# Optimization experiments

Hardware: AMD Instinct MI355X
Metric: run time of the kernel (lower is better)

The kernel has to match this reference:

```python
import jax, jax.numpy as jnp
import numpy as np

DIS_Z = 0.5     # depth search half-window (init kwarg dis_z)
NSAMPLE = 64    # max neighbors per query (init kwarg nsample)
B, N, M = 8, 16384, 2048


def setup_inputs() -> dict:
    key = jax.random.key(0)
    k1, k2 = jax.random.split(key)
    xyz1 = jax.random.normal(k1, (B, 3, N), dtype=jnp.float32)  # input points
    xyz2 = jax.random.normal(k2, (B, 3, M), dtype=jnp.float32)  # query points
    return {"xyz1": xyz1, "xyz2": xyz2}


def reference(xyz1, xyz2):
    """Depth-constrained radius search (semantics of query_depth_point CUDA kernel).

    For each query point q, scan input points j in order; if |z_j - z_q| < dis_z,
    record j. The first match pre-fills all nsample slots (ball-query convention),
    then subsequent matches overwrite slots 1..nsample-1. Stops after nsample
    matches. Returns idx (B,M,nsample) int64 and pts_cnt (B,M) int32.
    """
    n = xyz1.shape[2]
    z1 = xyz1[:, 2, :]                    # [B, N] input-point depths
    z2 = xyz2[:, 2, :]                    # [B, M] query-point depths
    # [B, M, N] depth-window mask (only the z coordinate is compared)
    mask = jnp.abs(z2[:, :, None] - z1[:, None, :]) < DIS_Z
    # Score earlier indices higher so top_k returns the FIRST nsample matches
    # in scan order; non-matches score 0.
    score = jnp.where(mask, n - jnp.arange(n, dtype=jnp.int32), 0)  # [B, M, N]
    vals, _ = jax.lax.top_k(score, NSAMPLE)   # [B, M, nsample], descending
    valid = vals > 0                          # slot k has a real (k-th) match
    idx_raw = n - vals                        # recover original index where valid
    first = idx_raw[..., 0:1]                 # index of first match (if any)
    cnt_total = jnp.sum(mask, axis=-1)        # [B, M] total matches
    pts_cnt = jnp.minimum(cnt_total, NSAMPLE).astype(jnp.int32)
    # Unfilled slots hold the first match index; if no match at all, stay 0.
    idx = jnp.where(valid, idx_raw,
                    jnp.where(cnt_total[..., None] > 0, first, 0)).astype(jnp.int64)
    return idx, pts_cnt
```

## Files before the change

kernel.cpp:

```cpp
#include <hip/hip_runtime.h>


#define QDP_B 8
#define QDP_N 16384
#define QDP_M 2048
#define QDP_NS 64
#define QDP_DISZ 0.5f

__global__ __launch_bounds__(256) void QueryDepthPoint_kernel(
    const float* __restrict__ xyz1,
    const float* __restrict__ xyz2,
    int* __restrict__ out_idx,
    int* __restrict__ out_cnt)
{
    const int lane = threadIdx.x & 63;
    const int wid  = (blockIdx.x << 2) + (threadIdx.x >> 6);

    const int b = wid >> 11;
    const int q = wid & (QDP_M - 1);

    const float zq = xyz2[b * 3 * QDP_M + 2 * QDP_M + q];
    const float* __restrict__ z1 = xyz1 + b * 3 * QDP_N + 2 * QDP_N;
    int* __restrict__ idx_out = out_idx + (size_t)wid * QDP_NS;

    int cnt    = 0;
    int firstv = 0;
    const unsigned long long below = (1ull << lane) - 1ull;

    const float* lptr = z1 + 8 * lane;
    float4 curA = ((const float4*)lptr)[0];
    float4 curB = ((const float4*)lptr)[1];

    for (int c = 0; c < QDP_N; c += 512) {
        const int pc = (c + 512 < QDP_N) ? (c + 512) : 0;
        const float* nptr = z1 + pc + 8 * lane;
        float4 nxtA = ((const float4*)nptr)[0];
        float4 nxtB = ((const float4*)nptr)[1];

        const bool m0 = fabsf(curA.x - zq) < QDP_DISZ;
        const bool m1 = fabsf(curA.y - zq) < QDP_DISZ;
        const bool m2 = fabsf(curA.z - zq) < QDP_DISZ;
        const bool m3 = fabsf(curA.w - zq) < QDP_DISZ;
        const bool m4 = fabsf(curB.x - zq) < QDP_DISZ;
        const bool m5 = fabsf(curB.y - zq) < QDP_DISZ;
        const bool m6 = fabsf(curB.z - zq) < QDP_DISZ;
        const bool m7 = fabsf(curB.w - zq) < QDP_DISZ;

        const unsigned long long b0 = __ballot(m0);
        const unsigned long long b1 = __ballot(m1);
        const unsigned long long b2 = __ballot(m2);
        const unsigned long long b3 = __ballot(m3);
        const unsigned long long b4 = __ballot(m4);
        const unsigned long long b5 = __ballot(m5);
        const unsigned long long b6 = __ballot(m6);
        const unsigned long long b7 = __ballot(m7);
        const unsigned long long any = b0|b1|b2|b3|b4|b5|b6|b7;

        if (any) {
            const int mbyte = (int)m0 | ((int)m1<<1) | ((int)m2<<2) | ((int)m3<<3)
                            | ((int)m4<<4) | ((int)m5<<5) | ((int)m6<<6) | ((int)m7<<7);
            if (cnt == 0) {
                const int l0  = (int)__builtin_ctzll(any);
                const int mb0 = __shfl(mbyte, l0);
                firstv = c + 8 * l0 + (int)__builtin_ctz((unsigned)mb0);
            }
            int r = cnt + __popcll(b0 & below) + __popcll(b1 & below)
                        + __popcll(b2 & below) + __popcll(b3 & below)
                        + __popcll(b4 & below) + __popcll(b5 & below)
                        + __popcll(b6 & below) + __popcll(b7 & below);
            const int base = c + 8 * lane;
            if (m0) { if (r < QDP_NS) idx_out[r] = base + 0; r++; }
            if (m1) { if (r < QDP_NS) idx_out[r] = base + 1; r++; }
            if (m2) { if (r < QDP_NS) idx_out[r] = base + 2; r++; }
            if (m3) { if (r < QDP_NS) idx_out[r] = base + 3; r++; }
            if (m4) { if (r < QDP_NS) idx_out[r] = base + 4; r++; }
            if (m5) { if (r < QDP_NS) idx_out[r] = base + 5; r++; }
            if (m6) { if (r < QDP_NS) idx_out[r] = base + 6; r++; }
            if (m7) { if (r < QDP_NS) idx_out[r] = base + 7; r++; }
            cnt += __popcll(b0) + __popcll(b1) + __popcll(b2) + __popcll(b3)
                 + __popcll(b4) + __popcll(b5) + __popcll(b6) + __popcll(b7);
            if (cnt >= QDP_NS) { cnt = QDP_NS; break; }
        }
        curA = nxtA; curB = nxtB;
    }

    if (lane >= cnt) idx_out[lane] = firstv;
    if (lane == 0)   out_cnt[wid] = cnt;
}

extern "C" void kernel_launch(void* const* d_in, const int* in_sizes, int n_in,
                              void* d_out, int out_size, void* d_ws, size_t ws_size,
                              hipStream_t stream) {
    const float* xyz1 = (const float*)d_in[0];
    const float* xyz2 = (const float*)d_in[1];
    int* out = (int*)d_out;

    int* out_idx = out;
    int* out_cnt = out + (size_t)QDP_B * QDP_M * QDP_NS;

    const int total_waves = QDP_B * QDP_M;
    const int grid = total_waves / 4;

    QueryDepthPoint_kernel<<<grid, 256, 0, stream>>>(xyz1, xyz2, out_idx, out_cnt);
}
```

Measured before the change: 72.76 us.

## Process sixteen queries per wavefront with a persistent grid and batched loads

Each wavefront now handles 16 consecutive queries in sequence instead of one. The grid shrinks to 256 blocks, and query depths are loaded once per wave and broadcast with shuffles. The scan loads four 512-element chunks per iteration before testing them, replacing the one-ahead prefetch. This cuts launch and wave setup overhead, but serializes queries within a wave and reduces parallelism to 1024 waves. That may leave the GPU underoccupied and expose load latency.

```diff
diff --git a/kernel.cpp b/kernel.cpp
--- a/kernel.cpp
+++ b/kernel.cpp
@@ -6,6 +6,56 @@
 #define QDP_M 2048
 #define QDP_NS 64
 #define QDP_DISZ 0.5f
+#define QDP_QPW 16
+
+__device__ __forceinline__ void qdp_group(
+    int cg, float zq, const float4& A, const float4& B,
+    int lane, unsigned long long below,
+    int& cnt, int& firstv, int* __restrict__ idx_out)
+{
+    const bool m0 = fabsf(A.x - zq) < QDP_DISZ;
+    const bool m1 = fabsf(A.y - zq) < QDP_DISZ;
+    const bool m2 = fabsf(A.z - zq) < QDP_DISZ;
+    const bool m3 = fabsf(A.w - zq) < QDP_DISZ;
+    const bool m4 = fabsf(B.x - zq) < QDP_DISZ;
+    const bool m5 = fabsf(B.y - zq) < QDP_DISZ;
+    const bool m6 = fabsf(B.z - zq) < QDP_DISZ;
+    const bool m7 = fabsf(B.w - zq) < QDP_DISZ;
+
+    const unsigned long long b0 = __ballot(m0);
+    const unsigned long long b1 = __ballot(m1);
+    const unsigned long long b2 = __ballot(m2);
+    const unsigned long long b3 = __ballot(m3);
+    const unsigned long long b4 = __ballot(m4);
+    const unsigned long long b5 = __ballot(m5);
+    const unsigned long long b6 = __ballot(m6);
+    const unsigned long long b7 = __ballot(m7);
+    const unsigned long long any = b0|b1|b2|b3|b4|b5|b6|b7;
+    if (!any) return;
+
+    const int mbyte = (int)m0 | ((int)m1<<1) | ((int)m2<<2) | ((int)m3<<3)
+                    | ((int)m4<<4) | ((int)m5<<5) | ((int)m6<<6) | ((int)m7<<7);
+    if (cnt == 0) {
+        const int l0  = (int)__builtin_ctzll(any);
+        const int mb0 = __shfl(mbyte, l0);
+        firstv = cg + 8 * l0 + (int)__builtin_ctz((unsigned)mb0);
+    }
+    int r = cnt + __popcll(b0 & below) + __popcll(b1 & below)
+                + __popcll(b2 & below) + __popcll(b3 & below)
+                + __popcll(b4 & below) + __popcll(b5 & below)
+                + __popcll(b6 & below) + __popcll(b7 & below);
+    const int base = cg + 8 * lane;
+    if (m0) { if (r < QDP_NS) idx_out[r] = base + 0; r++; }
+    if (m1) { if (r < QDP_NS) idx_out[r] = base + 1; r++; }
+    if (m2) { if (r < QDP_NS) idx_out[r] = base + 2; r++; }
+    if (m3) { if (r < QDP_NS) idx_out[r] = base + 3; r++; }
+    if (m4) { if (r < QDP_NS) idx_out[r] = base + 4; r++; }
+    if (m5) { if (r < QDP_NS) idx_out[r] = base + 5; r++; }
+    if (m6) { if (r < QDP_NS) idx_out[r] = base + 6; r++; }
+    if (m7) { if (r < QDP_NS) idx_out[r] = base + 7; r++; }
+    cnt += __popcll(b0) + __popcll(b1) + __popcll(b2) + __popcll(b3)
+         + __popcll(b4) + __popcll(b5) + __popcll(b6) + __popcll(b7);
+}
 
 __global__ __launch_bounds__(256) void QueryDepthPoint_kernel(
     const float* __restrict__ xyz1,
@@ -14,78 +64,48 @@
     int* __restrict__ out_cnt)
 {
     const int lane = threadIdx.x & 63;
-    const int wid  = (blockIdx.x << 2) + (threadIdx.x >> 6);
-
-    const int b = wid >> 11;
-    const int q = wid & (QDP_M - 1);
-
-    const float zq = xyz2[b * 3 * QDP_M + 2 * QDP_M + q];
-    const float* __restrict__ z1 = xyz1 + b * 3 * QDP_N + 2 * QDP_N;
-    int* __restrict__ idx_out = out_idx + (size_t)wid * QDP_NS;
-
-    int cnt    = 0;
-    int firstv = 0;
+    const int wv   = (blockIdx.x << 2) + (threadIdx.x >> 6);
     const unsigned long long below = (1ull << lane) - 1ull;
 
-    const float* lptr = z1 + 8 * lane;
-    float4 curA = ((const float4*)lptr)[0];
-    float4 curB = ((const float4*)lptr)[1];
+    const int qbase = wv * QDP_QPW;
+    const int b = qbase >> 11;
+    const float* __restrict__ z1 = xyz1 + b * 3 * QDP_N + 2 * QDP_N;
+    const float* __restrict__ z2 = xyz2 + b * 3 * QDP_M + 2 * QDP_M;
 
-    for (int c = 0; c < QDP_N; c += 512) {
-        const int pc = (c + 512 < QDP_N) ? (c + 512) : 0;
-        const float* nptr = z1 + pc + 8 * lane;
-        float4 nxtA = ((const float4*)nptr)[0];
-        float4 nxtB = ((const float4*)nptr)[1];
+    const float zqv = z2[(qbase & (QDP_M - 1)) + (lane & (QDP_QPW - 1))];
 
-        const bool m0 = fabsf(curA.x - zq) < QDP_DISZ;
-        const bool m1 = fabsf(curA.y - zq) < QDP_DISZ;
-        const bool m2 = fabsf(curA.z - zq) < QDP_DISZ;
-        const bool m3 = fabsf(curA.w - zq) < QDP_DISZ;
-        const bool m4 = fabsf(curB.x - zq) < QDP_DISZ;
-        const bool m5 = fabsf(curB.y - zq) < QDP_DISZ;
-        const bool m6 = fabsf(curB.z - zq) < QDP_DISZ;
-        const bool m7 = fabsf(curB.w - zq) < QDP_DISZ;
+    #pragma unroll 1
+    for (int k = 0; k < QDP_QPW; ++k) {
+        const float zq = __shfl(zqv, k);
+        int* __restrict__ idx_out = out_idx + (size_t)(qbase + k) * QDP_NS;
+        int cnt = 0, firstv = 0;
 
-        const unsigned long long b0 = __ballot(m0);
-        const unsigned long long b1 = __ballot(m1);
-        const unsigned long long b2 = __ballot(m2);
-        const unsigned long long b3 = __ballot(m3);
-        const unsigned long long b4 = __ballot(m4);
-        const unsigned long long b5 = __ballot(m5);
-        const unsigned long long b6 = __ballot(m6);
-        const unsigned long long b7 = __ballot(m7);
-        const unsigned long long any = b0|b1|b2|b3|b4|b5|b6|b7;
+        #pragma unroll 1
+        for (int c = 0; c < QDP_N; c += 2048) {
+            const float* p = z1 + c + 8 * lane;
+            const float4 a0 = ((const float4*)p)[0];
+            const float4 b0 = ((const float4*)p)[1];
+            const float4 a1 = ((const float4*)(p + 512))[0];
+            const float4 b1 = ((const float4*)(p + 512))[1];
+            const float4 a2 = ((const float4*)(p + 1024))[0];
+            const float4 b2 = ((const float4*)(p + 1024))[1];
+            const float4 a3 = ((const float4*)(p + 1536))[0];
+            const float4 b3 = ((const float4*)(p + 1536))[1];
 
-        if (any) {
-            const int mbyte = (int)m0 | ((int)m1<<1) | ((int)m2<<2) | ((int)m3<<3)
-                            | ((int)m4<<4) | ((int)m5<<5) | ((int)m6<<6) | ((int)m7<<7);
-            if (cnt == 0) {
-                const int l0  = (int)__builtin_ctzll(any);
-                const int mb0 = __shfl(mbyte, l0);
-                firstv = c + 8 * l0 + (int)__builtin_ctz((unsigned)mb0);
-            }
-            int r = cnt + __popcll(b0 & below) + __popcll(b1 & below)
-                        + __popcll(b2 & below) + __popcll(b3 & below)
-                        + __popcll(b4 & below) + __popcll(b5 & below)
-                        + __popcll(b6 & below) + __popcll(b7 & below);
-            const int base = c + 8 * lane;
-            if (m0) { if (r < QDP_NS) idx_out[r] = base + 0; r++; }
-            if (m1) { if (r < QDP_NS) idx_out[r] = base + 1; r++; }
-            if (m2) { if (r < QDP_NS) idx_out[r] = base + 2; r++; }
-            if (m3) { if (r < QDP_NS) idx_out[r] = base + 3; r++; }
-            if (m4) { if (r < QDP_NS) idx_out[r] = base + 4; r++; }
-            if (m5) { if (r < QDP_NS) idx_out[r] = base + 5; r++; }
-            if (m6) { if (r < QDP_NS) idx_out[r] = base + 6; r++; }
-            if (m7) { if (r < QDP_NS) idx_out[r] = base + 7; r++; }
-            cnt += __popcll(b0) + __popcll(b1) + __popcll(b2) + __popcll(b3)
-                 + __popcll(b4) + __popcll(b5) + __popcll(b6) + __popcll(b7);
-            if (cnt >= QDP_NS) { cnt = QDP_NS; break; }
+            qdp_group(c +    0, zq, a0, b0, lane, below, cnt, firstv, idx_out);
+            if (cnt >= QDP_NS) break;
+            qdp_group(c +  512, zq, a1, b1, lane, below, cnt, firstv, idx_out);
+            if (cnt >= QDP_NS) break;
+            qdp_group(c + 1024, zq, a2, b2, lane, below, cnt, firstv, idx_out);
+            if (cnt >= QDP_NS) break;
+            qdp_group(c + 1536, zq, a3, b3, lane, below, cnt, firstv, idx_out);
+            if (cnt >= QDP_NS) break;
         }
-        curA = nxtA; curB = nxtB;
+        if (cnt > QDP_NS) cnt = QDP_NS;
+
+        if (lane >= cnt) idx_out[lane] = firstv;
+        if (lane == 0)   out_cnt[qbase + k] = cnt;
     }
-
-    if (lane >= cnt) idx_out[lane] = firstv;
-    if (lane == 0)   out_cnt[wid] = cnt;
 }
 
 extern "C" void kernel_launch(void* const* d_in, const int* in_sizes, int n_in,
@@ -98,8 +118,5 @@
     int* out_idx = out;
     int* out_cnt = out + (size_t)QDP_B * QDP_M * QDP_NS;
 
-    const int total_waves = QDP_B * QDP_M;
-    const int grid = total_waves / 4;
-
-    QueryDepthPoint_kernel<<<grid, 256, 0, stream>>>(xyz1, xyz2, out_idx, out_cnt);
+    QueryDepthPoint_kernel<<<256, 256, 0, stream>>>(xyz1, xyz2, out_idx, out_cnt);
 }
```

Result: slower. 85.70 us (+17.8%).
